# Kernel tuning notes

Measured on AMD Instinct MI355X. Metric: run time of the kernel, lower is better.

## Reference

```python
import jax, jax.numpy as jnp
import numpy as np

D_MODEL = 1024
NUM_HEADS = 16
DEPTH = D_MODEL // NUM_HEADS
USE_MASKING = True


def setup_inputs() -> dict:
    key = jax.random.key(0)
    k1, k2, k3, k4 = jax.random.split(key, 4)
    B, S = 2, 2048
    x = jax.random.normal(k1, (B, S, D_MODEL), dtype=jnp.float32)
    # qkv_proj: Linear(d_model, 3*d_model, bias=False); torch stores W as [out, in]
    W_qkv = jax.random.normal(k2, (3 * D_MODEL, D_MODEL), dtype=jnp.float32) * (1.0 / np.sqrt(D_MODEL))
    W_out = jax.random.normal(k3, (D_MODEL, D_MODEL), dtype=jnp.float32) * (1.0 / np.sqrt(D_MODEL))
    b_out = jax.random.normal(k4, (D_MODEL,), dtype=jnp.float32) * 0.01
    return {"x": x, "W_qkv": W_qkv, "W_out": W_out, "b_out": b_out}


def reference(x, W_qkv, W_out, b_out):
    B, S, _ = x.shape
    qkv = jnp.einsum('bsd,ed->bse', x, W_qkv)  # [B,S,3*d_model]
    q, k, v = jnp.split(qkv, 3, axis=-1)
    # [B,S,H,depth] -> [B,H,S,depth]
    def heads(t):
        return t.reshape(B, S, NUM_HEADS, DEPTH).transpose(0, 2, 1, 3)
    q, k, v = heads(q), heads(k), heads(v)
    scores = jnp.einsum('bhqd,bhkd->bhqk', q, k) / np.sqrt(DEPTH).astype(np.float32)
    if USE_MASKING:
        mask = jnp.triu(jnp.ones((S, S), dtype=bool), k=1)
        scores = jnp.where(mask, -jnp.inf, scores)
    attn = jax.nn.softmax(scores, axis=-1)
    out = jnp.einsum('bhqk,bhkd->bhqd', attn, v)
    out = out.transpose(0, 2, 1, 3).reshape(B, S, D_MODEL)
    return jnp.einsum('bsd,ed->bse', out, W_out) + b_out
```

## Files before the change

kernel.cpp:

```cpp
#include <hip/hip_runtime.h>
#include <stdint.h>

typedef __attribute__((ext_vector_type(8))) short bf16x8;
typedef __attribute__((ext_vector_type(4))) float f32x4;
typedef __attribute__((ext_vector_type(4))) unsigned short u16x4;

#define AS1 __attribute__((address_space(1)))
#define AS3 __attribute__((address_space(3)))

#define BATCH 2
#define SEQ   2048
#define DMODEL 1024
#define NHEAD 16
#define DHEAD 64
#define QKVLD 3072
#define MROWS (BATCH*SEQ)

__device__ short g_xb   [MROWS * DMODEL];
__device__ short g_wqkv [3*DMODEL * DMODEL];
__device__ short g_wout [DMODEL * DMODEL];
__device__ short g_qkv  [(size_t)MROWS * QKVLD];
__device__ short g_attno[MROWS * DMODEL];

__device__ __forceinline__ unsigned short f2bf(float f) {
  union { float f; unsigned u; } v; v.f = f;
  unsigned r = v.u + 0x7FFFu + ((v.u >> 16) & 1u);
  return (unsigned short)(r >> 16);
}
__device__ __forceinline__ float bf2f(short s) {
  union { unsigned u; float f; } v; v.u = ((unsigned)(unsigned short)s) << 16;
  return v.f;
}
__device__ __forceinline__ void gload_lds16(const void* g, void* l) {
  __builtin_amdgcn_global_load_lds((const AS1 void*)(uintptr_t)g,
                                   (AS3 void*)(uint32_t)(uintptr_t)l, 16, 0, 0);
}

__global__ void cvt3(const float* __restrict__ x, const float* __restrict__ wq,
                     const float* __restrict__ wo) {
  const int N0 = MROWS * DMODEL;
  const int N1 = 3 * DMODEL * DMODEL;
  const int N2 = DMODEL * DMODEL;
  const int total = N0 + N1 + N2;
  int i = (blockIdx.x * blockDim.x + threadIdx.x) * 4;
  const int stride = gridDim.x * blockDim.x * 4;
  for (; i < total; i += stride) {
    const float* src; short* dst; int off;
    if (i < N0)           { src = x;  dst = g_xb;   off = i; }
    else if (i < N0 + N1) { src = wq; dst = g_wqkv; off = i - N0; }
    else                  { src = wo; dst = g_wout; off = i - N0 - N1; }
    float4 v = *reinterpret_cast<const float4*>(src + off);
    u16x4 o = { f2bf(v.x), f2bf(v.y), f2bf(v.z), f2bf(v.w) };
    *reinterpret_cast<u16x4*>(dst + off) = o;
  }
}

__device__ __forceinline__ void gemm_body(const short* __restrict__ A,
                                          const short* __restrict__ B,
                                          short* __restrict__ Cb,
                                          float* __restrict__ Cf,
                                          const float* __restrict__ bias,
                                          int N, int K) {
  __shared__ short As[128 * 32];
  __shared__ short Bs[128 * 32];
  const int tid  = threadIdx.x;
  const int lane = tid & 63;
  const int wid  = tid >> 6;
  const int wr = wid >> 1, wc = wid & 1;
  const int g = lane >> 4, c = lane & 15;
  const long row0 = (long)blockIdx.y * 128;
  const long col0 = (long)blockIdx.x * 128;

  const short* gA = A + (row0 + wid * 32 + (lane >> 2)) * (long)K + (lane & 3) * 8;
  const short* gB = B + (col0 + wid * 32 + (lane >> 2)) * (long)K + (lane & 3) * 8;
  short* lA = As + wid * 1024;
  short* lB = Bs + wid * 1024;

  f32x4 acc[4][4];
  const f32x4 z = {0.f, 0.f, 0.f, 0.f};
#pragma unroll
  for (int i = 0; i < 4; i++)
#pragma unroll
    for (int j = 0; j < 4; j++) acc[i][j] = z;

  for (int kt = 0; kt < K; kt += 32) {
    __syncthreads();
    gload_lds16(gA + kt,                lA);
    gload_lds16(gA + kt + 16 * (long)K, lA + 512);
    gload_lds16(gB + kt,                lB);
    gload_lds16(gB + kt + 16 * (long)K, lB + 512);
    __syncthreads();

    bf16x8 af[4], bfr[4];
#pragma unroll
    for (int mf = 0; mf < 4; mf++)
      af[mf] = *reinterpret_cast<const bf16x8*>(As + (wr * 64 + mf * 16 + c) * 32 + g * 8);
#pragma unroll
    for (int nf = 0; nf < 4; nf++)
      bfr[nf] = *reinterpret_cast<const bf16x8*>(Bs + (wc * 64 + nf * 16 + c) * 32 + g * 8);
#pragma unroll
    for (int mf = 0; mf < 4; mf++)
#pragma unroll
      for (int nf = 0; nf < 4; nf++)
        acc[mf][nf] = __builtin_amdgcn_mfma_f32_16x16x32_bf16(af[mf], bfr[nf], acc[mf][nf], 0, 0, 0);
  }

#pragma unroll
  for (int mf = 0; mf < 4; mf++)
#pragma unroll
    for (int nf = 0; nf < 4; nf++)
#pragma unroll
      for (int r = 0; r < 4; r++) {
        const long m = row0 + wr * 64 + mf * 16 + g * 4 + r;
        const long n = col0 + wc * 64 + nf * 16 + c;
        if (Cb) Cb[m * N + n] = (short)f2bf(acc[mf][nf][r]);
        else    Cf[m * N + n] = acc[mf][nf][r] + bias[n];
      }
}

__global__ __launch_bounds__(256) void gemm_qkv_k() {
  gemm_body(g_xb, g_wqkv, g_qkv, nullptr, nullptr, 3 * DMODEL, DMODEL);
}
__global__ __launch_bounds__(256) void gemm_out_k(float* __restrict__ out,
                                                  const float* __restrict__ bias) {
  gemm_body(g_attno, g_wout, nullptr, out, bias, DMODEL, DMODEL);
}

__global__ __launch_bounds__(256, 2) void flash_attn() {
  __shared__ short Kl[2][64 * 64];
  __shared__ short Vt[2][64 * 64];
  __shared__ short Pl[4][32 * 64];
  const int tid = threadIdx.x;
  const int lane = tid & 63, wid = tid >> 6;
  const int g = (lane >> 4) & 3, c = lane & 15;
  const int b = blockIdx.x >> 4, h = blockIdx.x & 15;
  const int qb = 15 - (int)blockIdx.y;
  const short* base = g_qkv + (size_t)b * SEQ * QKVLD + h * DHEAD;
  const int q0 = qb * 128;
  const int qw = q0 + wid * 32;
  const int nt = 2 * qb + 2;

  bf16x8 qf[2][2];
#pragma unroll
  for (int n = 0; n < 2; n++)
#pragma unroll
    for (int kc = 0; kc < 2; kc++) {
      bf16x8 raw = *reinterpret_cast<const bf16x8*>(
          base + (size_t)(qw + n * 16 + c) * QKVLD + kc * 32 + g * 8);
#pragma unroll
      for (int j = 0; j < 8; j++) raw[j] = (short)f2bf(bf2f(raw[j]) * 0.125f);
      qf[n][kc] = raw;
    }

  f32x4 oacc[2][4];
  const f32x4 z = {0.f, 0.f, 0.f, 0.f};
#pragma unroll
  for (int mq = 0; mq < 2; mq++)
#pragma unroll
    for (int nd = 0; nd < 4; nd++) oacc[mq][nd] = z;
  float mrow[2] = {-__builtin_inff(), -__builtin_inff()};
  float lrow[2] = {0.f, 0.f};

  const int srow = lane >> 3;
  const int scol = (lane & 7) ^ srow;
  const short* kgsrc = base + 1024 + (size_t)(wid * 16 + srow) * QKVLD + scol * 8;
  const short* vgsrc = base + 2048 + (size_t)lane * QKVLD + wid * 16;

  gload_lds16(kgsrc,                      &Kl[0][wid * 1024]);
  gload_lds16(kgsrc + (size_t)8 * QKVLD,  &Kl[0][wid * 1024 + 512]);
  {
    bf16x8 v0 = *reinterpret_cast<const bf16x8*>(vgsrc);
    bf16x8 v1 = *reinterpret_cast<const bf16x8*>(vgsrc + 8);
#pragma unroll
    for (int j = 0; j < 8; j++) {
      Vt[0][(wid * 16 + j) * 64 + (lane ^ (j << 3))] = v0[j];
      Vt[0][(wid * 16 + 8 + j) * 64 + (lane ^ (j << 3))] = v1[j];
    }
  }
  __syncthreads();

  for (int t = 0; t < nt; t++) {
    const int cur = t & 1;
    const int k0 = t * 64;
    const bool stage = (t + 1 < nt);
    bf16x8 vr0, vr1;
    if (stage) {
      const size_t roff = (size_t)(k0 + 64) * QKVLD;
      gload_lds16(kgsrc + roff,                     &Kl[cur ^ 1][wid * 1024]);
      gload_lds16(kgsrc + roff + (size_t)8 * QKVLD, &Kl[cur ^ 1][wid * 1024 + 512]);
      vr0 = *reinterpret_cast<const bf16x8*>(vgsrc + roff);
      vr1 = *reinterpret_cast<const bf16x8*>(vgsrc + roff + 8);
    }
    if (k0 <= qw + 31) {
      f32x4 sc[4][2];
#pragma unroll
      for (int m = 0; m < 4; m++) {
        const short* kr = &Kl[cur][(m * 16 + c) * 64];
        bf16x8 ka0 = *reinterpret_cast<const bf16x8*>(kr + ((g ^ (c & 7)) << 3));
        bf16x8 ka1 = *reinterpret_cast<const bf16x8*>(kr + (((4 + g) ^ (c & 7)) << 3));
#pragma unroll
        for (int n = 0; n < 2; n++) {
          f32x4 s = __builtin_amdgcn_mfma_f32_16x16x32_bf16(ka0, qf[n][0], z, 0, 0, 0);
          s = __builtin_amdgcn_mfma_f32_16x16x32_bf16(ka1, qf[n][1], s, 0, 0, 0);
          sc[m][n] = s;
        }
      }
      if (k0 + 63 > qw) {
#pragma unroll
        for (int m = 0; m < 4; m++)
#pragma unroll
          for (int n = 0; n < 2; n++)
#pragma unroll
            for (int r = 0; r < 4; r++)
              if (k0 + m * 16 + g * 4 + r > qw + n * 16 + c)
                sc[m][n][r] = -__builtin_inff();
      }
      float aln[2];
#pragma unroll
      for (int n = 0; n < 2; n++) {
        f32x4 mm0 = sc[0][n], mm1 = sc[1][n];
#pragma unroll
        for (int r = 0; r < 4; r++) {
          mm0[r] = fmaxf(mm0[r], sc[2][n][r]);
          mm1[r] = fmaxf(mm1[r], sc[3][n][r]);
        }
        float tm = fmaxf(fmaxf(fmaxf(mm0[0], mm0[1]), fmaxf(mm0[2], mm0[3])),
                         fmaxf(fmaxf(mm1[0], mm1[1]), fmaxf(mm1[2], mm1[3])));
        tm = fmaxf(tm, __shfl_xor(tm, 16, 64));
        tm = fmaxf(tm, __shfl_xor(tm, 32, 64));
        const float mn = fmaxf(mrow[n], tm);
        aln[n] = __expf(mrow[n] - mn);
        mrow[n] = mn;
        float rs = 0.f;
        const int q = n * 16 + c;
#pragma unroll
        for (int m = 0; m < 4; m++) {
          u16x4 pb;
#pragma unroll
          for (int r = 0; r < 4; r++) {
            const float p = __expf(sc[m][n][r] - mn);
            rs += p;
            pb[r] = f2bf(p);
          }
          const int idx = q * 64 + ((m * 16 + g * 4) ^ ((c & 7) << 3));
          *reinterpret_cast<u16x4*>(&Pl[wid][idx]) = pb;
        }
        rs += __shfl_xor(rs, 16, 64);
        rs += __shfl_xor(rs, 32, 64);
        lrow[n] = lrow[n] * aln[n] + rs;
      }
#pragma unroll
      for (int mq = 0; mq < 2; mq++)
#pragma unroll
        for (int r = 0; r < 4; r++) {
          const float alr = __shfl(aln[mq], g * 4 + r, 64);
#pragma unroll
          for (int nd = 0; nd < 4; nd++) oacc[mq][nd][r] *= alr;
        }
      asm volatile("s_waitcnt lgkmcnt(0)" ::: "memory");
      bf16x8 pa[2][2];
#pragma unroll
      for (int mq = 0; mq < 2; mq++) {
        const int q = mq * 16 + c;
#pragma unroll
        for (int kc = 0; kc < 2; kc++)
          pa[mq][kc] = *reinterpret_cast<const bf16x8*>(
              &Pl[wid][q * 64 + ((kc * 32 + g * 8) ^ ((c & 7) << 3))]);
      }
#pragma unroll
      for (int nd = 0; nd < 4; nd++) {
        const int d = nd * 16 + c;
#pragma unroll
        for (int kc = 0; kc < 2; kc++) {
          const bf16x8 vf = *reinterpret_cast<const bf16x8*>(
              &Vt[cur][d * 64 + ((kc * 32 + g * 8) ^ ((c & 7) << 3))]);
#pragma unroll
          for (int mq = 0; mq < 2; mq++)
            oacc[mq][nd] = __builtin_amdgcn_mfma_f32_16x16x32_bf16(pa[mq][kc], vf, oacc[mq][nd], 0, 0, 0);
        }
      }
    }
    if (stage) {
#pragma unroll
      for (int j = 0; j < 8; j++) {
        Vt[cur ^ 1][(wid * 16 + j) * 64 + (lane ^ (j << 3))] = vr0[j];
        Vt[cur ^ 1][(wid * 16 + 8 + j) * 64 + (lane ^ (j << 3))] = vr1[j];
      }
    }
    __syncthreads();
  }

  const float inv0 = 1.f / lrow[0], inv1 = 1.f / lrow[1];
#pragma unroll
  for (int mq = 0; mq < 2; mq++) {
    const float invm = mq ? inv1 : inv0;
#pragma unroll
    for (int r = 0; r < 4; r++) {
      const float linv = __shfl(invm, g * 4 + r, 64);
      const size_t orow = ((size_t)b * SEQ + qw + mq * 16 + g * 4 + r) * DMODEL + h * DHEAD;
#pragma unroll
      for (int nd = 0; nd < 4; nd++)
        g_attno[orow + nd * 16 + c] = (short)f2bf(oacc[mq][nd][r] * linv);
    }
  }
}

extern "C" void kernel_launch(void* const* d_in, const int* in_sizes, int n_in,
                              void* d_out, int out_size, void* d_ws, size_t ws_size,
                              hipStream_t stream) {
  (void)in_sizes; (void)n_in; (void)d_ws; (void)ws_size; (void)out_size;
  const float* x    = (const float*)d_in[0];
  const float* Wqkv = (const float*)d_in[1];
  const float* Wout = (const float*)d_in[2];
  const float* bout = (const float*)d_in[3];
  float* out = (float*)d_out;

  cvt3<<<2048, 256, 0, stream>>>(x, Wqkv, Wout);
  gemm_qkv_k<<<dim3(3 * DMODEL / 128, MROWS / 128), 256, 0, stream>>>();
  flash_attn<<<dim3(BATCH * NHEAD, SEQ / 128), 256, 0, stream>>>();
  gemm_out_k<<<dim3(DMODEL / 128, MROWS / 128), 256, 0, stream>>>(out, bout);
}
```

Before: 224.6 us.

## Triple-buffer attention K/V, add lazy rescale with exp2, swizzle GEMM and attention block order

The flash-attention kernel moves from double to triple buffering, prefetching K/V two tiles ahead and replacing __syncthreads with an explicit waitcnt plus s_barrier. Softmax switches to exp2 with log2e folded into the Q scale, and the running-max rescale is skipped unless the max grows by more than 8. MFMA sections get raised wave priority. Both GEMMs remap a 1D grid so groups of 8 blocks share row tiles for L2 reuse, and attention block ordering is reworked to pair long and short causal query tiles. Together these aim to hide load latency and cut exp/rescale ALU work, at the cost of more LDS per block (less occupancy headroom) and a looser softmax stability bound.

```diff
diff --git a/kernel.cpp b/kernel.cpp
--- a/kernel.cpp
+++ b/kernel.cpp
@@ -60,7 +60,7 @@
                                           short* __restrict__ Cb,
                                           float* __restrict__ Cf,
                                           const float* __restrict__ bias,
-                                          int N, int K) {
+                                          int N, int K, int bx, int by) {
   __shared__ short As[128 * 32];
   __shared__ short Bs[128 * 32];
   const int tid  = threadIdx.x;
@@ -68,8 +68,8 @@
   const int wid  = tid >> 6;
   const int wr = wid >> 1, wc = wid & 1;
   const int g = lane >> 4, c = lane & 15;
-  const long row0 = (long)blockIdx.y * 128;
-  const long col0 = (long)blockIdx.x * 128;
+  const long row0 = (long)by * 128;
+  const long col0 = (long)bx * 128;
 
   const short* gA = A + (row0 + wid * 32 + (lane >> 2)) * (long)K + (lane & 3) * 8;
   const short* gB = B + (col0 + wid * 32 + (lane >> 2)) * (long)K + (lane & 3) * 8;
@@ -119,27 +119,37 @@
 }
 
 __global__ __launch_bounds__(256) void gemm_qkv_k() {
-  gemm_body(g_xb, g_wqkv, g_qkv, nullptr, nullptr, 3 * DMODEL, DMODEL);
+  const int id = blockIdx.x;
+  const int j = id >> 3;
+  const int bx = j >> 2;
+  const int by = ((id & 7) << 2) | (j & 3);
+  gemm_body(g_xb, g_wqkv, g_qkv, nullptr, nullptr, 3 * DMODEL, DMODEL, bx, by);
 }
 __global__ __launch_bounds__(256) void gemm_out_k(float* __restrict__ out,
                                                   const float* __restrict__ bias) {
-  gemm_body(g_attno, g_wout, nullptr, out, bias, DMODEL, DMODEL);
+  const int id = blockIdx.x;
+  const int j = id >> 3;
+  const int bx = j >> 2;
+  const int by = ((id & 7) << 2) | (j & 3);
+  gemm_body(g_attno, g_wout, nullptr, out, bias, DMODEL, DMODEL, bx, by);
 }
 
 __global__ __launch_bounds__(256, 2) void flash_attn() {
-  __shared__ short Kl[2][64 * 64];
-  __shared__ short Vt[2][64 * 64];
+  __shared__ short Kl[3][64 * 64];
+  __shared__ short Vt[3][64 * 64];
   __shared__ short Pl[4][32 * 64];
   const int tid = threadIdx.x;
   const int lane = tid & 63, wid = tid >> 6;
   const int g = (lane >> 4) & 3, c = lane & 15;
-  const int b = blockIdx.x >> 4, h = blockIdx.x & 15;
-  const int qb = 15 - (int)blockIdx.y;
+  const int id = blockIdx.x;
+  const int bh = id & 31;
+  const int b = bh >> 4, h = bh & 15;
+  const int qb = (id < 256) ? (15 - (id >> 5)) : ((id - 256) >> 5);
   const short* base = g_qkv + (size_t)b * SEQ * QKVLD + h * DHEAD;
-  const int q0 = qb * 128;
-  const int qw = q0 + wid * 32;
+  const int qw = qb * 128 + wid * 32;
   const int nt = 2 * qb + 2;
 
+  const float QS = 0.18033688011112042f;
   bf16x8 qf[2][2];
 #pragma unroll
   for (int n = 0; n < 2; n++)
@@ -148,7 +158,7 @@
       bf16x8 raw = *reinterpret_cast<const bf16x8*>(
           base + (size_t)(qw + n * 16 + c) * QKVLD + kc * 32 + g * 8);
 #pragma unroll
-      for (int j = 0; j < 8; j++) raw[j] = (short)f2bf(bf2f(raw[j]) * 0.125f);
+      for (int j = 0; j < 8; j++) raw[j] = (short)f2bf(bf2f(raw[j]) * QS);
       qf[n][kc] = raw;
     }
 
@@ -166,33 +176,48 @@
   const short* kgsrc = base + 1024 + (size_t)(wid * 16 + srow) * QKVLD + scol * 8;
   const short* vgsrc = base + 2048 + (size_t)lane * QKVLD + wid * 16;
 
-  gload_lds16(kgsrc,                      &Kl[0][wid * 1024]);
-  gload_lds16(kgsrc + (size_t)8 * QKVLD,  &Kl[0][wid * 1024 + 512]);
   {
-    bf16x8 v0 = *reinterpret_cast<const bf16x8*>(vgsrc);
-    bf16x8 v1 = *reinterpret_cast<const bf16x8*>(vgsrc + 8);
+    bf16x8 a0 = *reinterpret_cast<const bf16x8*>(vgsrc);
+    bf16x8 a1 = *reinterpret_cast<const bf16x8*>(vgsrc + 8);
+    gload_lds16(kgsrc,                     &Kl[0][wid * 1024]);
+    gload_lds16(kgsrc + (size_t)8 * QKVLD, &Kl[0][wid * 1024 + 512]);
+    const size_t r1 = (size_t)64 * QKVLD;
+    bf16x8 b0 = *reinterpret_cast<const bf16x8*>(vgsrc + r1);
+    bf16x8 b1 = *reinterpret_cast<const bf16x8*>(vgsrc + r1 + 8);
+    gload_lds16(kgsrc + r1,                     &Kl[1][wid * 1024]);
+    gload_lds16(kgsrc + r1 + (size_t)8 * QKVLD, &Kl[1][wid * 1024 + 512]);
 #pragma unroll
     for (int j = 0; j < 8; j++) {
-      Vt[0][(wid * 16 + j) * 64 + (lane ^ (j << 3))] = v0[j];
-      Vt[0][(wid * 16 + 8 + j) * 64 + (lane ^ (j << 3))] = v1[j];
-    }
-  }
-  __syncthreads();
-
+      Vt[0][(wid * 16 + j) * 64 + (lane ^ (j << 3))] = a0[j];
+      Vt[0][(wid * 16 + 8 + j) * 64 + (lane ^ (j << 3))] = a1[j];
+    }
+#pragma unroll
+    for (int j = 0; j < 8; j++) {
+      Vt[1][(wid * 16 + j) * 64 + (lane ^ (j << 3))] = b0[j];
+      Vt[1][(wid * 16 + 8 + j) * 64 + (lane ^ (j << 3))] = b1[j];
+    }
+    asm volatile("s_waitcnt lgkmcnt(0)" ::: "memory");
+    __builtin_amdgcn_sched_barrier(0);
+    __builtin_amdgcn_s_barrier();
+    asm volatile("" ::: "memory");
+  }
+
+  int cur = 0;
   for (int t = 0; t < nt; t++) {
-    const int cur = t & 1;
-    const int k0 = t * 64;
-    const bool stage = (t + 1 < nt);
+    const int sidx = (cur + 2 >= 3) ? cur - 1 : cur + 2;
+    const bool sl = (t + 2 < nt);
     bf16x8 vr0, vr1;
-    if (stage) {
-      const size_t roff = (size_t)(k0 + 64) * QKVLD;
-      gload_lds16(kgsrc + roff,                     &Kl[cur ^ 1][wid * 1024]);
-      gload_lds16(kgsrc + roff + (size_t)8 * QKVLD, &Kl[cur ^ 1][wid * 1024 + 512]);
+    if (sl) {
+      const size_t roff = (size_t)(t + 2) * 64 * QKVLD;
       vr0 = *reinterpret_cast<const bf16x8*>(vgsrc + roff);
       vr1 = *reinterpret_cast<const bf16x8*>(vgsrc + roff + 8);
-    }
+      gload_lds16(kgsrc + roff,                     &Kl[sidx][wid * 1024]);
+      gload_lds16(kgsrc + roff + (size_t)8 * QKVLD, &Kl[sidx][wid * 1024 + 512]);
+    }
+    const int k0 = t * 64;
     if (k0 <= qw + 31) {
       f32x4 sc[4][2];
+      __builtin_amdgcn_s_setprio(1);
 #pragma unroll
       for (int m = 0; m < 4; m++) {
         const short* kr = &Kl[cur][(m * 16 + c) * 64];
@@ -205,6 +230,7 @@
           sc[m][n] = s;
         }
       }
+      __builtin_amdgcn_s_setprio(0);
       if (k0 + 63 > qw) {
 #pragma unroll
         for (int m = 0; m < 4; m++)
@@ -215,7 +241,7 @@
               if (k0 + m * 16 + g * 4 + r > qw + n * 16 + c)
                 sc[m][n][r] = -__builtin_inff();
       }
-      float aln[2];
+      float tm[2];
 #pragma unroll
       for (int n = 0; n < 2; n++) {
         f32x4 mm0 = sc[0][n], mm1 = sc[1][n];
@@ -224,13 +250,33 @@
           mm0[r] = fmaxf(mm0[r], sc[2][n][r]);
           mm1[r] = fmaxf(mm1[r], sc[3][n][r]);
         }
-        float tm = fmaxf(fmaxf(fmaxf(mm0[0], mm0[1]), fmaxf(mm0[2], mm0[3])),
-                         fmaxf(fmaxf(mm1[0], mm1[1]), fmaxf(mm1[2], mm1[3])));
-        tm = fmaxf(tm, __shfl_xor(tm, 16, 64));
-        tm = fmaxf(tm, __shfl_xor(tm, 32, 64));
-        const float mn = fmaxf(mrow[n], tm);
-        aln[n] = __expf(mrow[n] - mn);
-        mrow[n] = mn;
+        float v = fmaxf(fmaxf(fmaxf(mm0[0], mm0[1]), fmaxf(mm0[2], mm0[3])),
+                        fmaxf(fmaxf(mm1[0], mm1[1]), fmaxf(mm1[2], mm1[3])));
+        v = fmaxf(v, __shfl_xor(v, 16, 64));
+        v = fmaxf(v, __shfl_xor(v, 32, 64));
+        tm[n] = v;
+      }
+      const bool grow = (tm[0] > mrow[0] + 8.f) || (tm[1] > mrow[1] + 8.f);
+      if (__any(grow)) {
+        float aln[2];
+#pragma unroll
+        for (int n = 0; n < 2; n++) {
+          const float mn = fmaxf(mrow[n], tm[n]);
+          aln[n] = exp2f(mrow[n] - mn);
+          mrow[n] = mn;
+          lrow[n] *= aln[n];
+        }
+#pragma unroll
+        for (int mq = 0; mq < 2; mq++)
+#pragma unroll
+          for (int r = 0; r < 4; r++) {
+            const float alr = __shfl(aln[mq], g * 4 + r, 64);
+#pragma unroll
+            for (int nd = 0; nd < 4; nd++) oacc[mq][nd][r] *= alr;
+          }
+      }
+#pragma unroll
+      for (int n = 0; n < 2; n++) {
         float rs = 0.f;
         const int q = n * 16 + c;
 #pragma unroll
@@ -238,7 +284,7 @@
           u16x4 pb;
 #pragma unroll
           for (int r = 0; r < 4; r++) {
-            const float p = __expf(sc[m][n][r] - mn);
+            const float p = exp2f(sc[m][n][r] - mrow[n]);
             rs += p;
             pb[r] = f2bf(p);
           }
@@ -247,16 +293,8 @@
         }
         rs += __shfl_xor(rs, 16, 64);
         rs += __shfl_xor(rs, 32, 64);
-        lrow[n] = lrow[n] * aln[n] + rs;
-      }
-#pragma unroll
-      for (int mq = 0; mq < 2; mq++)
-#pragma unroll
-        for (int r = 0; r < 4; r++) {
-          const float alr = __shfl(aln[mq], g * 4 + r, 64);
-#pragma unroll
-          for (int nd = 0; nd < 4; nd++) oacc[mq][nd][r] *= alr;
-        }
+        lrow[n] += rs;
+      }
       asm volatile("s_waitcnt lgkmcnt(0)" ::: "memory");
       bf16x8 pa[2][2];
 #pragma unroll
@@ -267,6 +305,7 @@
           pa[mq][kc] = *reinterpret_cast<const bf16x8*>(
               &Pl[wid][q * 64 + ((kc * 32 + g * 8) ^ ((c & 7) << 3))]);
       }
+      __builtin_amdgcn_s_setprio(1);
 #pragma unroll
       for (int nd = 0; nd < 4; nd++) {
         const int d = nd * 16 + c;
@@ -279,15 +318,22 @@
             oacc[mq][nd] = __builtin_amdgcn_mfma_f32_16x16x32_bf16(pa[mq][kc], vf, oacc[mq][nd], 0, 0, 0);
         }
       }
-    }
-    if (stage) {
+      __builtin_amdgcn_s_setprio(0);
+    }
+    if (sl) {
 #pragma unroll
       for (int j = 0; j < 8; j++) {
-        Vt[cur ^ 1][(wid * 16 + j) * 64 + (lane ^ (j << 3))] = vr0[j];
-        Vt[cur ^ 1][(wid * 16 + 8 + j) * 64 + (lane ^ (j << 3))] = vr1[j];
-      }
-    }
-    __syncthreads();
+        Vt[sidx][(wid * 16 + j) * 64 + (lane ^ (j << 3))] = vr0[j];
+        Vt[sidx][(wid * 16 + 8 + j) * 64 + (lane ^ (j << 3))] = vr1[j];
+      }
+    } else {
+      asm volatile("s_waitcnt vmcnt(0)" ::: "memory");
+    }
+    asm volatile("s_waitcnt lgkmcnt(0)" ::: "memory");
+    __builtin_amdgcn_sched_barrier(0);
+    __builtin_amdgcn_s_barrier();
+    asm volatile("" ::: "memory");
+    cur = (cur + 1 == 3) ? 0 : cur + 1;
   }
 
   const float inv0 = 1.f / lrow[0], inv1 = 1.f / lrow[1];
@@ -316,7 +362,7 @@
   float* out = (float*)d_out;
 
   cvt3<<<2048, 256, 0, stream>>>(x, Wqkv, Wout);
-  gemm_qkv_k<<<dim3(3 * DMODEL / 128, MROWS / 128), 256, 0, stream>>>();
-  flash_attn<<<dim3(BATCH * NHEAD, SEQ / 128), 256, 0, stream>>>();
-  gemm_out_k<<<dim3(DMODEL / 128, MROWS / 128), 256, 0, stream>>>(out, bout);
-}
+  gemm_qkv_k<<<768, 256, 0, stream>>>();
+  flash_attn<<<512, 256, 0, stream>>>();
+  gemm_out_k<<<256, 256, 0, stream>>>(out, bout);
+}
```

Result: faster. 217.7 us (-3.0%).
